# Performance work log

Hardware: AMD Instinct MI355X
Metric: run time of the kernel (lower is better)

Reference implementation:

```python
import jax, jax.numpy as jnp
import numpy as np

B, S, D, H, O, E, K = 4, 2048, 1024, 2048, 1024, 8, 2

def setup_inputs() -> dict:
    key = jax.random.key(0)
    ks = jax.random.split(key, 8)
    x = jax.random.normal(ks[0], (B, S, D), dtype=jnp.float32)
    # kaiming-uniform-ish scale for weights, zero biases (as in _init_w)
    gate_w = jax.random.uniform(ks[1], (E, D), dtype=jnp.float32, minval=-1, maxval=1) * np.sqrt(6.0 / D)
    gate_b = jnp.zeros((E,), dtype=jnp.float32)
    w1 = jax.random.uniform(ks[2], (E, D, H), dtype=jnp.float32, minval=-1, maxval=1) * np.sqrt(6.0 / D)
    b1 = jnp.zeros((E, H), dtype=jnp.float32)
    w2 = jax.random.uniform(ks[3], (E, H, O), dtype=jnp.float32, minval=-1, maxval=1) * np.sqrt(6.0 / H)
    b2 = jnp.zeros((E, O), dtype=jnp.float32)
    return {"x": x, "gate_w": gate_w, "gate_b": gate_b, "w1": w1, "b1": b1, "w2": w2, "b2": b2}

def reference(x, gate_w, gate_b, w1, b1, w2, b2):
    # gate: softmax over experts, then top-k (k=2)
    logits = jnp.einsum('bsd,ed->bse', x, gate_w) + gate_b          # [B,S,E]
    probs = jax.nn.softmax(logits, axis=-1)
    topk_vals, topk_idx = jax.lax.top_k(probs, K)                    # [B,S,K]
    # dense all-expert MLPs (Linear-ReLU-Linear), dropout = 0
    h = jax.nn.relu(jnp.einsum('bsd,edh->bseh', x, w1) + b1)         # [B,S,E,H]
    expert_out = jnp.einsum('bseh,eho->bseo', h, w2) + b2            # [B,S,E,O]
    # gather top-k experts and combine with gate weights
    sel = jnp.take_along_axis(expert_out, topk_idx[..., None], axis=2)  # [B,S,K,O]
    return jnp.sum(sel * topk_vals[..., None], axis=2)               # [B,S,O]
```

## Files before the change

### kernel.cpp

```cpp
#include <hip/hip_runtime.h>

#define T_TOKENS 8192
#define D_DIM 1024
#define H_DIM 2048
#define O_DIM 1024
#define E_NUM 8
#define NPAIR 16384

typedef unsigned short u16;
typedef __bf16 bf16x8 __attribute__((ext_vector_type(8)));
typedef float f32x4 __attribute__((ext_vector_type(4)));

__device__ inline u16 f2bf(float f) {
  union { float f; unsigned u; } v; v.f = f;
  unsigned r = v.u + 0x7FFFu + ((v.u >> 16) & 1u);
  return (u16)(r >> 16);
}

__device__ __forceinline__ void gload16(const u16* g, u16* l) {
  __builtin_amdgcn_global_load_lds((const __attribute__((address_space(1))) void*)g,
                                   (__attribute__((address_space(3))) void*)l, 16, 0, 0);
}

__global__ void transpose_cvt_kernel(const float* __restrict__ w, u16* __restrict__ wt,
                                     int R, int C) {
  __shared__ float tile[32][33];
  int e = blockIdx.z;
  int c0 = blockIdx.x * 32, r0 = blockIdx.y * 32;
  const float* wp = w + (size_t)e * R * C;
  u16* wtp = wt + (size_t)e * R * C;
  int tx = threadIdx.x, ty = threadIdx.y;
  #pragma unroll
  for (int j = 0; j < 32; j += 8)
    tile[ty + j][tx] = wp[(size_t)(r0 + ty + j) * C + c0 + tx];
  __syncthreads();
  #pragma unroll
  for (int j = 0; j < 32; j += 8)
    wtp[(size_t)(c0 + ty + j) * R + r0 + tx] = f2bf(tile[tx][ty + j]);
}

__global__ void gate_kernel(const float* __restrict__ x, const float* __restrict__ gw,
                            const float* __restrict__ gb, int* __restrict__ topk_idx,
                            float* __restrict__ topk_val, u16* __restrict__ xb) {
  int t = blockIdx.x * 4 + (threadIdx.x >> 6);
  int lane = threadIdx.x & 63;
  const float4* xr4 = (const float4*)(x + (size_t)t * D_DIM);
  const float4* gw4 = (const float4*)gw;
  u16* xbr = xb + (size_t)t * D_DIM;
  float acc[E_NUM];
  #pragma unroll
  for (int e = 0; e < E_NUM; e++) acc[e] = 0.f;
  #pragma unroll
  for (int it = 0; it < D_DIM / 256; ++it) {
    float4 xv = xr4[it * 64 + lane];
    ushort4 o;
    o.x = f2bf(xv.x); o.y = f2bf(xv.y); o.z = f2bf(xv.z); o.w = f2bf(xv.w);
    *(ushort4*)(xbr + (it * 64 + lane) * 4) = o;
    #pragma unroll
    for (int e = 0; e < E_NUM; e++) {
      float4 wv = gw4[e * (D_DIM / 4) + it * 64 + lane];
      acc[e] += xv.x * wv.x + xv.y * wv.y + xv.z * wv.z + xv.w * wv.w;
    }
  }
  #pragma unroll
  for (int e = 0; e < E_NUM; e++) {
    #pragma unroll
    for (int o = 32; o > 0; o >>= 1) acc[e] += __shfl_down(acc[e], o);
  }
  if (lane == 0) {
    float l[E_NUM], mx = -1e30f;
    #pragma unroll
    for (int e = 0; e < E_NUM; e++) { l[e] = acc[e] + gb[e]; mx = fmaxf(mx, l[e]); }
    float p[E_NUM], s = 0.f;
    #pragma unroll
    for (int e = 0; e < E_NUM; e++) { p[e] = expf(l[e] - mx); s += p[e]; }
    float inv = 1.f / s;
    int i1 = 0;
    #pragma unroll
    for (int e = 1; e < E_NUM; e++) if (p[e] > p[i1]) i1 = e;
    int i2 = (i1 == 0) ? 1 : 0;
    #pragma unroll
    for (int e = 0; e < E_NUM; e++) if (e != i1 && e != i2 && p[e] > p[i2]) i2 = e;
    topk_idx[t * 2] = i1;     topk_idx[t * 2 + 1] = i2;
    topk_val[t * 2] = p[i1] * inv; topk_val[t * 2 + 1] = p[i2] * inv;
  }
}

__global__ void histscan_kernel(const int* __restrict__ topk_idx,
                                int* __restrict__ counts, int* __restrict__ eoff) {
  __shared__ int wh[4][E_NUM];
  int tid = threadIdx.x;
  int lane = tid & 63, wave = tid >> 6;
  int myc = 0;
  for (int i = tid; i < NPAIR; i += 256) {
    int e = topk_idx[i];
    #pragma unroll
    for (int ee = 0; ee < E_NUM; ee++) {
      unsigned long long m = __ballot(e == ee);
      if (lane == ee) myc += __popcll(m);
    }
  }
  if (lane < E_NUM) wh[wave][lane] = myc;
  __syncthreads();
  if (tid == 0) {
    int s = 0;
    for (int e = 0; e < E_NUM; e++) {
      int c = wh[0][e] + wh[1][e] + wh[2][e] + wh[3][e];
      counts[e] = c;
      eoff[e] = s;
      s += c;
    }
    eoff[E_NUM] = s;
  }
}

__global__ void scatter_kernel(const int* __restrict__ topk_idx, const float* __restrict__ topk_val,
                               const int* __restrict__ eoff, int* __restrict__ cursor_pad,
                               int* __restrict__ pair_token, float* __restrict__ pair_gate) {
  __shared__ int lhist[E_NUM];
  __shared__ int lbase[E_NUM];
  int tid = threadIdx.x;
  int t = blockIdx.x * 256 + tid;
  if (tid < E_NUM) lhist[tid] = 0;
  __syncthreads();
  int e0 = topk_idx[t * 2], e1 = topk_idx[t * 2 + 1];
  int r0 = atomicAdd(&lhist[e0], 1);
  int r1 = atomicAdd(&lhist[e1], 1);
  __syncthreads();
  if (tid < E_NUM) lbase[tid] = eoff[tid] + atomicAdd(&cursor_pad[tid * 32], lhist[tid]);
  __syncthreads();
  int p0 = lbase[e0] + r0;
  int p1 = lbase[e1] + r1;
  pair_token[p0] = t; pair_gate[p0] = topk_val[t * 2];
  pair_token[p1] = t; pair_gate[p1] = topk_val[t * 2 + 1];
}


__global__ __launch_bounds__(256, 3) void gemm1_kernel(
    const u16* __restrict__ xb, const u16* __restrict__ w1t, const float* __restrict__ b1,
    const int* __restrict__ pair_token, const int* __restrict__ eoff,
    const int* __restrict__ ecnt, u16* __restrict__ hbuf) {
  const int e = blockIdx.z;
  const int ne = ecnt[e];
  const int m0t = blockIdx.y * 128;
  if (m0t >= ne) return;
  const int off = eoff[e];
  const int n0 = blockIdx.x * 128;

  __shared__ __align__(16) u16 As[128 * 64];
  __shared__ __align__(16) u16 Bs[128 * 64];

  const int tid = threadIdx.x;
  const int wid = tid >> 6;
  const int lane = tid & 63;

  const int strow8 = lane >> 3;
  const int slot = lane & 7;
  const u16* aptr[4]; const u16* bptr[4];
  u16* lA[4]; u16* lB[4];
  #pragma unroll
  for (int j = 0; j < 4; j++) {
    int r = wid * 32 + j * 8 + strow8;
    int gm = m0t + r;
    int tok = (gm < ne) ? pair_token[off + gm] : 0;
    int gl = slot ^ (r & 7);
    aptr[j] = xb + (size_t)tok * D_DIM + gl * 8;
    bptr[j] = w1t + ((size_t)e * H_DIM + (n0 + r)) * D_DIM + gl * 8;
    lA[j] = As + wid * 2048 + j * 512;
    lB[j] = Bs + wid * 2048 + j * 512;
  }

  const int wm = (wid & 1) * 64;
  const int wn = (wid >> 1) * 64;
  const int lrow = lane & 15;
  const int quad = lane >> 4;
  const int pg0 = quad ^ (lrow & 7);
  const int pg1 = (quad + 4) ^ (lrow & 7);

  f32x4 acc[4][4] = {};

  for (int k0 = 0; k0 < D_DIM; k0 += 64) {
    #pragma unroll
    for (int j = 0; j < 4; j++) { gload16(aptr[j] + k0, lA[j]); gload16(bptr[j] + k0, lB[j]); }
    __syncthreads();
    {
      bf16x8 af[4], bfr[4];
      #pragma unroll
      for (int i = 0; i < 4; i++) af[i] = *(const bf16x8*)&As[(wm + i * 16 + lrow) * 64 + pg0 * 8];
      #pragma unroll
      for (int j = 0; j < 4; j++) bfr[j] = *(const bf16x8*)&Bs[(wn + j * 16 + lrow) * 64 + pg0 * 8];
      #pragma unroll
      for (int i = 0; i < 4; i++)
        #pragma unroll
        for (int j = 0; j < 4; j++)
          acc[i][j] = __builtin_amdgcn_mfma_f32_16x16x32_bf16(af[i], bfr[j], acc[i][j], 0, 0, 0);
    }
    {
      bf16x8 af[4], bfr[4];
      #pragma unroll
      for (int i = 0; i < 4; i++) af[i] = *(const bf16x8*)&As[(wm + i * 16 + lrow) * 64 + pg1 * 8];
      #pragma unroll
      for (int j = 0; j < 4; j++) bfr[j] = *(const bf16x8*)&Bs[(wn + j * 16 + lrow) * 64 + pg1 * 8];
      #pragma unroll
      for (int i = 0; i < 4; i++)
        #pragma unroll
        for (int j = 0; j < 4; j++)
          acc[i][j] = __builtin_amdgcn_mfma_f32_16x16x32_bf16(af[i], bfr[j], acc[i][j], 0, 0, 0);
    }
    __syncthreads();
  }
  #pragma unroll
  for (int i = 0; i < 4; i++) {
    #pragma unroll
    for (int r = 0; r < 4; r++) {
      int m = wm + i * 16 + quad * 4 + r;
      int gm = m0t + m;
      if (gm >= ne) continue;
      size_t rowbase = (size_t)(off + gm) * H_DIM;
      #pragma unroll
      for (int j = 0; j < 4; j++) {
        int n = n0 + wn + j * 16 + lrow;
        float v = acc[i][j][r] + b1[e * H_DIM + n];
        v = v > 0.f ? v : 0.f;
        hbuf[rowbase + n] = f2bf(v);
      }
    }
  }
}

__global__ __launch_bounds__(256, 3) void gemm2_kernel(
    const u16* __restrict__ hbuf, const u16* __restrict__ w2t, const float* __restrict__ b2,
    const int* __restrict__ pair_token, const float* __restrict__ pair_gate,
    const int* __restrict__ eoff, const int* __restrict__ ecnt, float* __restrict__ out) {
  const int e = blockIdx.z;
  const int ne = ecnt[e];
  const int m0t = blockIdx.y * 128;
  if (m0t >= ne) return;
  const int off = eoff[e];
  const int n0 = blockIdx.x * 128;

  __shared__ __align__(16) u16 As[128 * 64];
  __shared__ __align__(16) u16 Bs[128 * 64];

  const int tid = threadIdx.x;
  const int wid = tid >> 6;
  const int lane = tid & 63;

  const int strow8 = lane >> 3;
  const int slot = lane & 7;
  const u16* aptr[4]; const u16* bptr[4];
  u16* lA[4]; u16* lB[4];
  #pragma unroll
  for (int j = 0; j < 4; j++) {
    int r = wid * 32 + j * 8 + strow8;
    int gl = slot ^ (r & 7);
    aptr[j] = hbuf + (size_t)(off + m0t + r) * H_DIM + gl * 8;
    bptr[j] = w2t + ((size_t)e * O_DIM + (n0 + r)) * H_DIM + gl * 8;
    lA[j] = As + wid * 2048 + j * 512;
    lB[j] = Bs + wid * 2048 + j * 512;
  }

  const int wm = (wid & 1) * 64;
  const int wn = (wid >> 1) * 64;
  const int lrow = lane & 15;
  const int quad = lane >> 4;
  const int pg0 = quad ^ (lrow & 7);
  const int pg1 = (quad + 4) ^ (lrow & 7);

  f32x4 acc[4][4] = {};

  for (int k0 = 0; k0 < H_DIM; k0 += 64) {
    #pragma unroll
    for (int j = 0; j < 4; j++) { gload16(aptr[j] + k0, lA[j]); gload16(bptr[j] + k0, lB[j]); }
    __syncthreads();
    {
      bf16x8 af[4], bfr[4];
      #pragma unroll
      for (int i = 0; i < 4; i++) af[i] = *(const bf16x8*)&As[(wm + i * 16 + lrow) * 64 + pg0 * 8];
      #pragma unroll
      for (int j = 0; j < 4; j++) bfr[j] = *(const bf16x8*)&Bs[(wn + j * 16 + lrow) * 64 + pg0 * 8];
      #pragma unroll
      for (int i = 0; i < 4; i++)
        #pragma unroll
        for (int j = 0; j < 4; j++)
          acc[i][j] = __builtin_amdgcn_mfma_f32_16x16x32_bf16(af[i], bfr[j], acc[i][j], 0, 0, 0);
    }
    {
      bf16x8 af[4], bfr[4];
      #pragma unroll
      for (int i = 0; i < 4; i++) af[i] = *(const bf16x8*)&As[(wm + i * 16 + lrow) * 64 + pg1 * 8];
      #pragma unroll
      for (int j = 0; j < 4; j++) bfr[j] = *(const bf16x8*)&Bs[(wn + j * 16 + lrow) * 64 + pg1 * 8];
      #pragma unroll
      for (int i = 0; i < 4; i++)
        #pragma unroll
        for (int j = 0; j < 4; j++)
          acc[i][j] = __builtin_amdgcn_mfma_f32_16x16x32_bf16(af[i], bfr[j], acc[i][j], 0, 0, 0);
    }
    __syncthreads();
  }
  #pragma unroll
  for (int i = 0; i < 4; i++) {
    #pragma unroll
    for (int r = 0; r < 4; r++) {
      int m = wm + i * 16 + quad * 4 + r;
      int gm = m0t + m;
      if (gm >= ne) continue;
      int pair = off + gm;
      int tok = pair_token[pair];
      float g = pair_gate[pair];
      #pragma unroll
      for (int j = 0; j < 4; j++) {
        int n = n0 + wn + j * 16 + lrow;
        float v = (acc[i][j][r] + b2[e * O_DIM + n]) * g;
        atomicAdd(&out[(size_t)tok * O_DIM + n], v);
      }
    }
  }
}

extern "C" void kernel_launch(void* const* d_in, const int* in_sizes, int n_in,
                              void* d_out, int out_size, void* d_ws, size_t ws_size,
                              hipStream_t stream) {
  const float* x  = (const float*)d_in[0];
  const float* gw = (const float*)d_in[1];
  const float* gb = (const float*)d_in[2];
  const float* w1 = (const float*)d_in[3];
  const float* b1 = (const float*)d_in[4];
  const float* w2 = (const float*)d_in[5];
  const float* b2 = (const float*)d_in[6];
  float* out = (float*)d_out;

  char* ws = (char*)d_ws;
  size_t off = 0;
  auto take = [&](size_t bytes) -> char* {
    char* p = ws + off;
    off = (off + bytes + 255) & ~(size_t)255;
    return p;
  };
  int*   meta       = (int*)take(2048);
  int*   cursor_pad = meta;
  int*   counts     = meta + 256;
  int*   eoff       = meta + 264;
  int*   topk_idx   = (int*)take((size_t)T_TOKENS * 2 * 4);
  float* topk_val   = (float*)take((size_t)T_TOKENS * 2 * 4);
  int*   pair_token = (int*)take((size_t)(NPAIR + 256) * 4);
  float* pair_gate  = (float*)take((size_t)(NPAIR + 256) * 4);
  u16*   xb         = (u16*)take((size_t)T_TOKENS * D_DIM * 2);
  u16*   w1t        = (u16*)take((size_t)E_NUM * D_DIM * H_DIM * 2);
  u16*   w2t        = (u16*)take((size_t)E_NUM * H_DIM * O_DIM * 2);
  u16*   hbuf       = (u16*)take((size_t)(NPAIR + 128) * H_DIM * 2);

  hipMemsetAsync(meta, 0, 2048, stream);
  hipMemsetAsync(out, 0, (size_t)T_TOKENS * O_DIM * 4, stream);

  transpose_cvt_kernel<<<dim3(H_DIM / 32, D_DIM / 32, E_NUM), dim3(32, 8), 0, stream>>>(w1, w1t, D_DIM, H_DIM);
  transpose_cvt_kernel<<<dim3(O_DIM / 32, H_DIM / 32, E_NUM), dim3(32, 8), 0, stream>>>(w2, w2t, H_DIM, O_DIM);
  gate_kernel<<<T_TOKENS / 4, 256, 0, stream>>>(x, gw, gb, topk_idx, topk_val, xb);
  histscan_kernel<<<1, 256, 0, stream>>>(topk_idx, counts, eoff);
  scatter_kernel<<<T_TOKENS / 256, 256, 0, stream>>>(topk_idx, topk_val, eoff, cursor_pad, pair_token, pair_gate);
  gemm1_kernel<<<dim3(H_DIM / 128, NPAIR / 128, E_NUM), 256, 0, stream>>>(xb, w1t, b1, pair_token, eoff, counts, hbuf);
  gemm2_kernel<<<dim3(O_DIM / 128, NPAIR / 128, E_NUM), 256, 0, stream>>>(hbuf, w2t, b2, pair_token, pair_gate, eoff, counts, out);
}
```

Measured before the change: 493.9 us.

## Load GEMM operands directly from global into registers, dropping LDS staging

```diff
diff --git a/kernel.cpp b/kernel.cpp
--- a/kernel.cpp
+++ b/kernel.cpp
@@ -15,11 +15,6 @@
   union { float f; unsigned u; } v; v.f = f;
   unsigned r = v.u + 0x7FFFu + ((v.u >> 16) & 1u);
   return (u16)(r >> 16);
-}
-
-__device__ __forceinline__ void gload16(const u16* g, u16* l) {
-  __builtin_amdgcn_global_load_lds((const __attribute__((address_space(1))) void*)g,
-                                   (__attribute__((address_space(3))) void*)l, 16, 0, 0);
 }
 
 __global__ void transpose_cvt_kernel(const float* __restrict__ w, u16* __restrict__ wt,
@@ -136,7 +131,7 @@
 }
 
 
-__global__ __launch_bounds__(256, 3) void gemm1_kernel(
+__global__ __launch_bounds__(256, 2) void gemm1_kernel(
     const u16* __restrict__ xb, const u16* __restrict__ w1t, const float* __restrict__ b1,
     const int* __restrict__ pair_token, const int* __restrict__ eoff,
     const int* __restrict__ ecnt, u16* __restrict__ hbuf) {
@@ -147,67 +142,49 @@
   const int off = eoff[e];
   const int n0 = blockIdx.x * 128;
 
-  __shared__ __align__(16) u16 As[128 * 64];
-  __shared__ __align__(16) u16 Bs[128 * 64];
-
   const int tid = threadIdx.x;
   const int wid = tid >> 6;
   const int lane = tid & 63;
-
-  const int strow8 = lane >> 3;
-  const int slot = lane & 7;
-  const u16* aptr[4]; const u16* bptr[4];
-  u16* lA[4]; u16* lB[4];
-  #pragma unroll
-  for (int j = 0; j < 4; j++) {
-    int r = wid * 32 + j * 8 + strow8;
-    int gm = m0t + r;
-    int tok = (gm < ne) ? pair_token[off + gm] : 0;
-    int gl = slot ^ (r & 7);
-    aptr[j] = xb + (size_t)tok * D_DIM + gl * 8;
-    bptr[j] = w1t + ((size_t)e * H_DIM + (n0 + r)) * D_DIM + gl * 8;
-    lA[j] = As + wid * 2048 + j * 512;
-    lB[j] = Bs + wid * 2048 + j * 512;
-  }
-
   const int wm = (wid & 1) * 64;
   const int wn = (wid >> 1) * 64;
   const int lrow = lane & 15;
   const int quad = lane >> 4;
-  const int pg0 = quad ^ (lrow & 7);
-  const int pg1 = (quad + 4) ^ (lrow & 7);
+
+  const u16* Ab[4];
+  #pragma unroll
+  for (int i = 0; i < 4; i++) {
+    int gm = m0t + wm + i * 16 + lrow;
+    int tok = (gm < ne) ? pair_token[off + gm] : 0;
+    Ab[i] = xb + (size_t)tok * D_DIM + quad * 8;
+  }
+  const u16* Bb[4];
+  #pragma unroll
+  for (int j = 0; j < 4; j++) {
+    int n = n0 + wn + j * 16 + lrow;
+    Bb[j] = w1t + ((size_t)e * H_DIM + n) * D_DIM + quad * 8;
+  }
 
   f32x4 acc[4][4] = {};
-
-  for (int k0 = 0; k0 < D_DIM; k0 += 64) {
-    #pragma unroll
-    for (int j = 0; j < 4; j++) { gload16(aptr[j] + k0, lA[j]); gload16(bptr[j] + k0, lB[j]); }
-    __syncthreads();
-    {
-      bf16x8 af[4], bfr[4];
-      #pragma unroll
-      for (int i = 0; i < 4; i++) af[i] = *(const bf16x8*)&As[(wm + i * 16 + lrow) * 64 + pg0 * 8];
-      #pragma unroll
-      for (int j = 0; j < 4; j++) bfr[j] = *(const bf16x8*)&Bs[(wn + j * 16 + lrow) * 64 + pg0 * 8];
-      #pragma unroll
-      for (int i = 0; i < 4; i++)
-        #pragma unroll
-        for (int j = 0; j < 4; j++)
-          acc[i][j] = __builtin_amdgcn_mfma_f32_16x16x32_bf16(af[i], bfr[j], acc[i][j], 0, 0, 0);
-    }
-    {
-      bf16x8 af[4], bfr[4];
-      #pragma unroll
-      for (int i = 0; i < 4; i++) af[i] = *(const bf16x8*)&As[(wm + i * 16 + lrow) * 64 + pg1 * 8];
-      #pragma unroll
-      for (int j = 0; j < 4; j++) bfr[j] = *(const bf16x8*)&Bs[(wn + j * 16 + lrow) * 64 + pg1 * 8];
-      #pragma unroll
-      for (int i = 0; i < 4; i++)
-        #pragma unroll
-        for (int j = 0; j < 4; j++)
-          acc[i][j] = __builtin_amdgcn_mfma_f32_16x16x32_bf16(af[i], bfr[j], acc[i][j], 0, 0, 0);
-    }
-    __syncthreads();
+  bf16x8 af[2][4], bfr[2][4];
+  #pragma unroll
+  for (int i = 0; i < 4; i++) af[0][i] = *(const bf16x8*)(Ab[i]);
+  #pragma unroll
+  for (int j = 0; j < 4; j++) bfr[0][j] = *(const bf16x8*)(Bb[j]);
+
+  for (int k0 = 0; k0 < D_DIM; k0 += 32) {
+    int cb = (k0 >> 5) & 1;
+    int kn = k0 + 32;
+    if (kn < D_DIM) {
+      #pragma unroll
+      for (int i = 0; i < 4; i++) af[cb ^ 1][i] = *(const bf16x8*)(Ab[i] + kn);
+      #pragma unroll
+      for (int j = 0; j < 4; j++) bfr[cb ^ 1][j] = *(const bf16x8*)(Bb[j] + kn);
+    }
+    #pragma unroll
+    for (int i = 0; i < 4; i++)
+      #pragma unroll
+      for (int j = 0; j < 4; j++)
+        acc[i][j] = __builtin_amdgcn_mfma_f32_16x16x32_bf16(af[cb][i], bfr[cb][j], acc[i][j], 0, 0, 0);
   }
   #pragma unroll
   for (int i = 0; i < 4; i++) {
@@ -228,7 +205,7 @@
   }
 }
 
-__global__ __launch_bounds__(256, 3) void gemm2_kernel(
+__global__ __launch_bounds__(256, 2) void gemm2_kernel(
     const u16* __restrict__ hbuf, const u16* __restrict__ w2t, const float* __restrict__ b2,
     const int* __restrict__ pair_token, const float* __restrict__ pair_gate,
     const int* __restrict__ eoff, const int* __restrict__ ecnt, float* __restrict__ out) {
@@ -239,65 +216,48 @@
   const int off = eoff[e];
   const int n0 = blockIdx.x * 128;
 
-  __shared__ __align__(16) u16 As[128 * 64];
-  __shared__ __align__(16) u16 Bs[128 * 64];
-
   const int tid = threadIdx.x;
   const int wid = tid >> 6;
   const int lane = tid & 63;
-
-  const int strow8 = lane >> 3;
-  const int slot = lane & 7;
-  const u16* aptr[4]; const u16* bptr[4];
-  u16* lA[4]; u16* lB[4];
-  #pragma unroll
-  for (int j = 0; j < 4; j++) {
-    int r = wid * 32 + j * 8 + strow8;
-    int gl = slot ^ (r & 7);
-    aptr[j] = hbuf + (size_t)(off + m0t + r) * H_DIM + gl * 8;
-    bptr[j] = w2t + ((size_t)e * O_DIM + (n0 + r)) * H_DIM + gl * 8;
-    lA[j] = As + wid * 2048 + j * 512;
-    lB[j] = Bs + wid * 2048 + j * 512;
-  }
-
   const int wm = (wid & 1) * 64;
   const int wn = (wid >> 1) * 64;
   const int lrow = lane & 15;
   const int quad = lane >> 4;
-  const int pg0 = quad ^ (lrow & 7);
-  const int pg1 = (quad + 4) ^ (lrow & 7);
+
+  const u16* Ab[4];
+  #pragma unroll
+  for (int i = 0; i < 4; i++) {
+    int gm = m0t + wm + i * 16 + lrow;
+    Ab[i] = hbuf + (size_t)(off + gm) * H_DIM + quad * 8;
+  }
+  const u16* Bb[4];
+  #pragma unroll
+  for (int j = 0; j < 4; j++) {
+    int n = n0 + wn + j * 16 + lrow;
+    Bb[j] = w2t + ((size_t)e * O_DIM + n) * H_DIM + quad * 8;
+  }
 
   f32x4 acc[4][4] = {};
-
-  for (int k0 = 0; k0 < H_DIM; k0 += 64) {
-    #pragma unroll
-    for (int j = 0; j < 4; j++) { gload16(aptr[j] + k0, lA[j]); gload16(bptr[j] + k0, lB[j]); }
-    __syncthreads();
-    {
-      bf16x8 af[4], bfr[4];
-      #pragma unroll
-      for (int i = 0; i < 4; i++) af[i] = *(const bf16x8*)&As[(wm + i * 16 + lrow) * 64 + pg0 * 8];
-      #pragma unroll
-      for (int j = 0; j < 4; j++) bfr[j] = *(const bf16x8*)&Bs[(wn + j * 16 + lrow) * 64 + pg0 * 8];
-      #pragma unroll
-      for (int i = 0; i < 4; i++)
-        #pragma unroll
-        for (int j = 0; j < 4; j++)
-          acc[i][j] = __builtin_amdgcn_mfma_f32_16x16x32_bf16(af[i], bfr[j], acc[i][j], 0, 0, 0);
-    }
-    {
-      bf16x8 af[4], bfr[4];
-      #pragma unroll
-      for (int i = 0; i < 4; i++) af[i] = *(const bf16x8*)&As[(wm + i * 16 + lrow) * 64 + pg1 * 8];
-      #pragma unroll
-      for (int j = 0; j < 4; j++) bfr[j] = *(const bf16x8*)&Bs[(wn + j * 16 + lrow) * 64 + pg1 * 8];
-      #pragma unroll
-      for (int i = 0; i < 4; i++)
-        #pragma unroll
-        for (int j = 0; j < 4; j++)
-          acc[i][j] = __builtin_amdgcn_mfma_f32_16x16x32_bf16(af[i], bfr[j], acc[i][j], 0, 0, 0);
-    }
-    __syncthreads();
+  bf16x8 af[2][4], bfr[2][4];
+  #pragma unroll
+  for (int i = 0; i < 4; i++) af[0][i] = *(const bf16x8*)(Ab[i]);
+  #pragma unroll
+  for (int j = 0; j < 4; j++) bfr[0][j] = *(const bf16x8*)(Bb[j]);
+
+  for (int k0 = 0; k0 < H_DIM; k0 += 32) {
+    int cb = (k0 >> 5) & 1;
+    int kn = k0 + 32;
+    if (kn < H_DIM) {
+      #pragma unroll
+      for (int i = 0; i < 4; i++) af[cb ^ 1][i] = *(const bf16x8*)(Ab[i] + kn);
+      #pragma unroll
+      for (int j = 0; j < 4; j++) bfr[cb ^ 1][j] = *(const bf16x8*)(Bb[j] + kn);
+    }
+    #pragma unroll
+    for (int i = 0; i < 4; i++)
+      #pragma unroll
+      for (int j = 0; j < 4; j++)
+        acc[i][j] = __builtin_amdgcn_mfma_f32_16x16x32_bf16(af[cb][i], bfr[cb][j], acc[i][j], 0, 0, 0);
   }
   #pragma unroll
   for (int i = 0; i < 4; i++) {
```

Result: slower. 889.7 us (+80.1%).
